# Optimization experiments

Measured on AMD Instinct MI355X. Metric: run time of the kernel, lower is better.

Reference implementation:

```python
import jax, jax.numpy as jnp
import numpy as np
import math

B, T = 8, 16
CODE_NUM = 1024
CODE_SIZE = 48
GRAPH_SIZE = 32
HIDDEN = 150      # hidden_size == t_output_size
T_ATTN = 32       # t_attention_size
DP_ATTN = 32      # DotProductAttention size
OUT = 1024


def _lin(k, fan_in, fan_out):
    s = 1.0 / math.sqrt(fan_in)
    kw, kb = jax.random.split(k)
    W = jax.random.uniform(kw, (fan_in, fan_out), minval=-s, maxval=s, dtype=jnp.float32)
    b = jax.random.uniform(kb, (fan_out,), minval=-s, maxval=s, dtype=jnp.float32)
    return W, b


def setup_inputs():
    key = jax.random.key(0)
    ks = jax.random.split(key, 16)
    u = jax.random.uniform(ks[0], (B, T, CODE_NUM))
    m1 = (u < 0.03).astype(jnp.float32)                   # persistent codes
    m2 = ((u >= 0.03) & (u < 0.05)).astype(jnp.float32)   # emerging neighbor codes
    m3 = ((u >= 0.05) & (u < 0.06)).astype(jnp.float32)   # emerging unrelated codes
    divided = jnp.stack([m1, m2, m3], axis=-1)            # [B,T,N,3], disjoint
    code_x = jnp.clip(m1 + m2 + m3, 0.0, 1.0)             # current-visit codes
    neighbors = ((u >= 0.06) & (u < 0.12)).astype(jnp.float32)
    lens = jax.random.randint(ks[1], (B,), T // 2, T + 1)
    a = (jax.random.uniform(ks[2], (CODE_NUM, CODE_NUM)) < 0.01).astype(jnp.float32)
    adj = a / (a.sum(axis=1, keepdims=True) + 1e-6)
    c_emb = jax.random.normal(ks[3], (CODE_NUM, CODE_SIZE)) * 0.05
    n_emb = jax.random.normal(ks[4], (CODE_NUM, CODE_SIZE)) * 0.05
    u_emb = jax.random.normal(ks[5], (CODE_NUM, GRAPH_SIZE)) * 0.05
    Wg, bg = _lin(ks[6], CODE_SIZE, GRAPH_SIZE)           # GraphLayer dense
    Wi, bi = _lin(ks[7], GRAPH_SIZE, 3 * HIDDEN)          # GRUCell input (r|z|n)
    Wh, bh = _lin(ks[8], HIDDEN, 3 * HIDDEN)              # GRUCell hidden (r|z|n)
    Wq, bq = _lin(ks[9], GRAPH_SIZE, T_ATTN)
    Wk, bk = _lin(ks[10], GRAPH_SIZE, T_ATTN)
    Wv, bv = _lin(ks[11], GRAPH_SIZE, HIDDEN)
    Wd, bd = _lin(ks[12], HIDDEN, DP_ATTN)                # DotProductAttention dense
    context = jax.random.normal(ks[13], (DP_ATTN,)) * 0.1
    Wc, bc = _lin(ks[14], HIDDEN, OUT)                    # Classifier
    return dict(code_x=code_x, divided=divided, neighbors=neighbors, lens=lens,
                adj=adj, c_emb=c_emb, n_emb=n_emb, u_emb=u_emb, Wg=Wg, bg=bg,
                Wi=Wi, bi=bi, Wh=Wh, bh=bh, Wq=Wq, bq=bq, Wk=Wk, bk=bk,
                Wv=Wv, bv=bv, Wd=Wd, bd=bd, context=context, Wc=Wc, bc=bc)


def _forward(code_x, divided, neighbors, lens, adj, c_emb, n_emb, u_emb,
             Wg, bg, Wi, bi, Wh, bh, Wq, bq, Wk, bk, Wv, bv, Wd, bd, context, Wc, bc):
    Bb, Tt, N = code_x.shape
    H = Wh.shape[0]
    NEG = -1e30
    scale = 1.0 / math.sqrt(Wq.shape[1])

    def step(carry, xs):
        h_prev, no_prev = carry                 # [B,N,H], [B,N,G]
        c_t, d_t, n_t, t_idx = xs               # [B,N], [B,N,3], [B,N], scalar
        c = c_t[..., None]
        nb = n_t[..., None]
        # GraphLayer: masked embeddings + one-hop adjacency aggregation
        ce = c * c_emb                           # [B,N,C]
        ne = nb * n_emb
        adj_ce = jnp.einsum('mn,bnc->bmc', adj, ce)
        adj_ne = jnp.einsum('mn,bnc->bmc', adj, ne)
        co = jax.nn.leaky_relu((ce + c * adj_ce + c * adj_ne) @ Wg + bg)      # [B,N,G]
        no = jax.nn.leaky_relu((ne + nb * adj_ne + nb * adj_ce) @ Wg + bg)

        m1 = d_t[..., 0]; m2 = d_t[..., 1]; m3 = d_t[..., 2]
        # TransitionLayer part 1: GRUCell on persistent (m1) codes; h_new starts at 0
        gi = co @ Wi + bi
        gh = h_prev @ Wh + bh
        i_r, i_z, i_n = jnp.split(gi, 3, axis=-1)
        h_r, h_z, h_n = jnp.split(gh, 3, axis=-1)
        r = jax.nn.sigmoid(i_r + h_r)
        z = jax.nn.sigmoid(i_z + h_z)
        n_g = jnp.tanh(i_n + r * h_n)
        h_m1 = (1.0 - z) * n_g + z * h_prev
        h_new = jnp.where(m1[..., None] > 0, h_m1, 0.0)

        # TransitionLayer part 2: single-head attention over emerging (m2|m3) codes, t>0
        m23 = (m2 + m3) > 0
        qrows = jnp.where(m2[..., None] > 0, no_prev,
                          jnp.where(m3[..., None] > 0, u_emb, 0.0))           # [B,N,G]
        q = qrows @ Wq + bq
        k = co @ Wk + bk
        v = qrows @ Wv + bv
        s = jnp.einsum('bia,bja->bij', q, k) * scale
        s = jnp.where(m23[:, None, :], s, NEG)   # keys restricted to m2|m3 set
        h_m23 = jnp.tanh(jnp.einsum('bij,bjh->bih', jax.nn.softmax(s, axis=-1), v))
        use23 = t_idx > 0
        h_new = jnp.where(jnp.logical_and(use23, m23)[..., None], h_m23, h_new)

        # per-step output: max-pool over each active subset (0 if subset empty)
        om1 = jnp.max(jnp.where(m1[..., None] > 0, h_m1, NEG), axis=1)
        om1 = jnp.where(jnp.any(m1 > 0, axis=1)[:, None], om1, 0.0)
        om23 = jnp.max(jnp.where(m23[..., None], h_m23, NEG), axis=1)
        om23 = jnp.where(jnp.logical_and(use23, jnp.any(m23, axis=1))[:, None], om23, 0.0)
        return (h_new, no), om1 + om23

    h0 = jnp.zeros((Bb, N, H), code_x.dtype)
    no0 = jnp.zeros((Bb, N, Wg.shape[1]), code_x.dtype)
    xs = (jnp.moveaxis(code_x, 1, 0), jnp.moveaxis(divided, 1, 0),
          jnp.moveaxis(neighbors, 1, 0), jnp.arange(Tt))
    _, outs = jax.lax.scan(step, (h0, no0), xs)
    outs = jnp.moveaxis(outs, 0, 1)              # [B,T,H]

    # DotProductAttention over (ragged) visit axis
    vu = (outs @ Wd + bd) @ context              # [B,T]
    tmask = jnp.arange(Tt)[None, :] < lens[:, None]
    score = jax.nn.softmax(jnp.where(tmask, vu, NEG), axis=-1)
    pooled = jnp.einsum('bth,bt->bh', outs, score)
    # Classifier (dropout_rate=0 -> identity) with sigmoid activation
    return jax.nn.sigmoid(pooled @ Wc + bc)


def reference(code_x, divided, neighbors, lens, adj, c_emb, n_emb, u_emb,
              Wg, bg, Wi, bi, Wh, bh, Wq, bq, Wk, bk, Wv, bv, Wd, bd, context, Wc, bc):
    return _forward(code_x, divided, neighbors, lens, adj, c_emb, n_emb, u_emb,
                    Wg, bg, Wi, bi, Wh, bh, Wq, bq, Wk, bk, Wv, bv, Wd, bd,
                    context, Wc, bc)
```

## Files before the change

kernel.cpp:

```cpp
#include <hip/hip_runtime.h>

#define Bq   8
#define Tq   16
#define Nq   1024
#define Cq   48
#define Gq   32
#define Hq   150
#define H3q  450
#define TAq  32
#define OUTq 1024
#define BTq  128
#define NBLK (2 * BTq)
#define THREADS 512

#define NC_CAP 128
#define NM_CAP 64
#define NACT   (2 * NC_CAP)
#define MTILE  16
#define NMH    (NM_CAP / 2)
#define CHUNK  16

__device__ __forceinline__ float lrelu(float x){ return x > 0.f ? x : 0.01f * x; }
__device__ __forceinline__ float sigm(float x){ return 1.f / (1.f + expf(-x)); }

__device__ __align__(16) int   g_n1[BTq], g_n23[BTq], g_nchain[BTq], g_nchain2[BTq];
__device__ __align__(16) int   g_list1[BTq][NM_CAP];
__device__ __align__(16) int   g_list23[BTq][NM_CAP];
__device__ __align__(16) int   g_mapc[BTq][Nq];
__device__ __align__(16) int   g_mapn[BTq][Nq];
__device__ __align__(16) int   g_chain[BTq][NM_CAP];
__device__ __align__(16) int   g_chain2[BTq][NM_CAP];
__device__ __align__(16) int   g_cls[BTq][NM_CAP];
__device__ __align__(16) float g_co[BTq][NC_CAP][Gq];
__device__ __align__(16) float g_no[BTq][NC_CAP][Gq];
__device__ __align__(16) float g_hm23[BTq][NM_CAP][Hq];
__device__ __align__(16) float g_om23p2[2][BTq][Hq];
__device__ __align__(16) float g_hm1[BTq][NM_CAP][Hq];
__device__ __align__(16) float g_om1p2[2][BTq][Hq];
__device__ __align__(16) float g_om1c[BTq][Hq];

template<typename T>
__device__ __forceinline__ T gld(const T* p){
    return __hip_atomic_load(p, __ATOMIC_RELAXED, __HIP_MEMORY_SCOPE_AGENT);
}
template<typename T>
__device__ __forceinline__ void gst(T* p, T v){
    __hip_atomic_store(p, v, __ATOMIC_RELAXED, __HIP_MEMORY_SCOPE_AGENT);
}

__device__ unsigned int g_done[NBLK][16];

__device__ __forceinline__ void publish(unsigned int val){
    asm volatile("s_waitcnt vmcnt(0)" ::: "memory");
    __syncthreads();
    if (threadIdx.x == 0)
        __hip_atomic_store(&g_done[blockIdx.x][0], val,
                           __ATOMIC_RELAXED, __HIP_MEMORY_SCOPE_AGENT);
}

__device__ __forceinline__ void spin_ge(int b2, unsigned int tgt){
    while ((int)(__hip_atomic_load(&g_done[b2][0],
                                   __ATOMIC_RELAXED, __HIP_MEMORY_SCOPE_AGENT) - tgt) < 0)
        __builtin_amdgcn_s_sleep(4);
}

__device__ __forceinline__ void gi3(const float* co_row, const float* Wi, const float* bi, int h,
                                    float& gr, float& gz, float& gn){
    gr = bi[h]; gz = bi[Hq + h]; gn = bi[2 * Hq + h];
    #pragma unroll
    for (int g = 0; g < Gq; ++g){
        float c = co_row[g];
        const float* w = Wi + g * H3q + h;
        gr += c * w[0];
        gz += c * w[Hq];
        gn += c * w[2 * Hq];
    }
}

#define WARM(ptr, nfloats) { int nv_ = (nfloats) >> 2; \
    for (int i4_ = blk * THREADS + tid; i4_ < nv_; i4_ += NBLK * THREADS){ \
        float4 v_ = ((const float4*)(ptr))[i4_]; \
        wacc += v_.x + v_.y + v_.z + v_.w; } }

union SharedU {
    struct {
        unsigned char cf[Nq], nf[Nq];
        short lc[NC_CAP], ln[NC_CAP];
        short act[NACT];
        float Wg[Cq][Gq];
        float Pact[NACT][Gq];
        float A[MTILE][NACT];
    } co;
    struct {
        unsigned char f1[Nq], f2[Nq], f3[Nq];
        short l1[NM_CAP], l23[NM_CAP];
        unsigned char wm[NMH];
        float co23[NM_CAP][Gq];
        float qr[NM_CAP][Gq];
        float q[NMH][TAq + 1];
        float k[NM_CAP][TAq + 1];
        float s[NMH][NM_CAP + 1];
        float vv[NM_CAP][Hq];
        float hm[NMH][Hq];
    } mid;
    struct {
        short map1p[Nq], map23p[Nq];
        short l1[NM_CAP];
        unsigned char cls[NM_CAP];
        int   m23l[NM_CAP];
        float co1[NMH][Gq];
        float hb[Hq];
        float ghf[H3q];
        float gi[NMH][H3q];
    } g1;
    struct {
        int   proc[NM_CAP];
        float hb[CHUNK][Hq];
        float co[CHUNK][Gq];
        float ghf[CHUNK][H3q];
        float hm[CHUNK][Hq];
        float cmax[Hq];
    } g1b;
    struct {
        int   nch2[Tq];
        float co[Gq];
        float hb[Hq];
        float ghf[H3q];
        float outs[Tq][Hq];
        float wdc[Hq];
        float score[Tq];
        float pooled[Hq];
        float cpart[32][17];
    } fin;
};

#define CO_PREFETCH(P, kk) { int rbase_ = half + (kk) * 2 * MTILE; \
    int ntile_ = min(MTILE, (total - rbase_ + 1) / 2); int lim_ = ntile_ * total; \
    _Pragma("unroll") for (int u = 0; u < 8; ++u){ int idx_ = tid + u * THREADS; \
        if (idx_ < lim_){ int ti_ = idx_ / total, j_ = idx_ - ti_ * total; \
            P[u] = adj[(size_t)sh.co.act[rbase_ + 2 * ti_] * Nq + sh.co.act[j_]]; } } }

#define CO_STORE(P, kk) { int rbase_ = half + (kk) * 2 * MTILE; \
    int ntile_ = min(MTILE, (total - rbase_ + 1) / 2); int lim_ = ntile_ * total; \
    _Pragma("unroll") for (int u = 0; u < 8; ++u){ int idx_ = tid + u * THREADS; \
        if (idx_ < lim_){ int ti_ = idx_ / total, j_ = idx_ - ti_ * total; \
            sh.co.A[ti_][j_] = P[u]; } } }

#define CO_COMPUTE(kk) { int rbase_ = half + (kk) * 2 * MTILE; \
    int ntile_ = min(MTILE, (total - rbase_ + 1) / 2); \
    if (grp < ntile_){ int r_ = rbase_ + 2 * grp; float agg_ = 0.f; \
        _Pragma("unroll 4") for (int j_ = 0; j_ < total; ++j_) \
            agg_ += sh.co.A[grp][j_] * sh.co.Pact[j_][g]; \
        float v_ = lrelu(sh.co.Pact[r_][g] + agg_ + bgv); \
        if (r_ < nc) gst(&g_co[bt][r_][g], v_); else gst(&g_no[bt][r_ - nc][g], v_); } }

__global__ __launch_bounds__(THREADS, 1) void k_fused(
    const float* code_x, const float* divided, const float* neighbors,
    const int* lens, const float* adj, const float* c_emb, const float* n_emb,
    const float* u_emb, const float* Wg, const float* bg,
    const float* Wi, const float* bi, const float* Wh, const float* bh,
    const float* Wq_, const float* bq_, const float* Wk_, const float* bk_,
    const float* Wv_, const float* bv_, const float* Wd, const float* bd,
    const float* ctx, const float* Wc, const float* bc, float* out)
{
    __shared__ SharedU sh;
    __shared__ int s_n0, s_n1v, s_i2;
    const int tid = threadIdx.x;
    const int blk = blockIdx.x;
    const int bt   = blk >> 1;
    const int half = blk & 1;
    const int t    = bt % Tq;
    const int btp  = bt - 1;
    const unsigned int bar0 = __hip_atomic_load(&g_done[blk][0],
                                                __ATOMIC_RELAXED, __HIP_MEMORY_SCOPE_AGENT);

    float wacc = 0.f;
    WARM(code_x,    BTq * Nq);
    WARM(neighbors, BTq * Nq);
    WARM(adj,       Nq * Nq);
    WARM(divided,   BTq * Nq * 3);
    WARM(c_emb,     Nq * Cq);
    WARM(n_emb,     Nq * Cq);
    WARM(u_emb,     Nq * Gq);
    WARM(Wi,        Gq * H3q);
    WARM(Wh,        Hq * H3q);
    WARM(Wc,        Hq * OUTq);
    WARM(Wv_,       Gq * Hq);
    WARM(Wd,        Hq * TAq);

    {
        int wave = tid >> 6, lane = tid & 63;
        for (int n = tid; n < Nq; n += THREADS){
            sh.co.cf[n] = (code_x[bt * Nq + n]    > 0.f) ? 1 : 0;
            sh.co.nf[n] = (neighbors[bt * Nq + n] > 0.f) ? 1 : 0;
        }
        for (int i = tid; i < Cq * Gq; i += THREADS) (&sh.co.Wg[0][0])[i] = Wg[i];
        __syncthreads();
        if (wave == 0){
            int base = 0;
            for (int start = 0; start < Nq; start += 64){
                int n = start + lane;
                int pred = sh.co.cf[n];
                unsigned long long mm = __ballot(pred != 0);
                int pos = base + (int)__popcll(mm & ((1ull << lane) - 1ull));
                if (pred && pos < NC_CAP) sh.co.lc[pos] = (short)n;
                base += (int)__popcll(mm);
            }
            if (lane == 0) s_n0 = min(base, NC_CAP);
        } else if (wave == 1){
            int base = 0;
            for (int start = 0; start < Nq; start += 64){
                int n = start + lane;
                int pred = sh.co.nf[n];
                unsigned long long mm = __ballot(pred != 0);
                int pos = base + (int)__popcll(mm & ((1ull << lane) - 1ull));
                if (pred && pos < NC_CAP) sh.co.ln[pos] = (short)n;
                base += (int)__popcll(mm);
            }
            if (lane == 0) s_n1v = min(base, NC_CAP);
        } else {
            if (half == 0) for (int n = tid - 128; n < Nq; n += 384) gst(&g_mapc[bt][n], -1);
            else           for (int n = tid - 128; n < Nq; n += 384) gst(&g_mapn[bt][n], -1);
        }
        __syncthreads();
        int nc = s_n0, nn = s_n1v, total = nc + nn;

        for (int i = tid; i < total; i += THREADS) sh.co.act[i] = (i < nc) ? sh.co.lc[i] : sh.co.ln[i - nc];
        if (half == 0) for (int i = tid; i < nc; i += THREADS) gst(&g_mapc[bt][sh.co.lc[i]], i);
        else           for (int i = tid; i < nn; i += THREADS) gst(&g_mapn[bt][sh.co.ln[i]], i);
        __syncthreads();

        for (int idx = tid; idx < total * Gq; idx += THREADS){
            int i = idx >> 5, g = idx & 31;
            int row = sh.co.act[i];
            const float* e = (i < nc) ? (c_emb + row * Cq) : (n_emb + row * Cq);
            float acc = 0.f;
            #pragma unroll
            for (int c = 0; c < Cq; ++c) acc += e[c] * sh.co.Wg[c][g];
            sh.co.Pact[i][g] = acc;
        }
        __syncthreads();

        int g = tid & 31, grp = tid >> 5;
        float bgv = bg[g];
        int ntiles = (total > half) ? (total - half + 2 * MTILE - 1) / (2 * MTILE) : 0;
        float pA[8], pB[8];
        if (ntiles > 0) CO_PREFETCH(pA, 0);
        for (int k = 0; k < ntiles; ){
            CO_STORE(pA, k);
            __syncthreads();
            if (k + 1 < ntiles) CO_PREFETCH(pB, k + 1);
            CO_COMPUTE(k);
            __syncthreads();
            ++k; if (k >= ntiles) break;
            CO_STORE(pB, k);
            __syncthreads();
            if (k + 1 < ntiles) CO_PREFETCH(pA, k + 1);
            CO_COMPUTE(k);
            __syncthreads();
            ++k;
        }
    }
    asm volatile("" :: "v"(wacc));
    publish(bar0 + 1);
    float dv[6];
    #pragma unroll
    for (int u = 0; u < 6; ++u) dv[u] = divided[(size_t)bt * (Nq * 3) + tid + u * THREADS];
    if (tid == 0) spin_ge(blk ^ 1, bar0 + 1);
    else if (t > 0 && tid == 1) spin_ge(2 * btp,     bar0 + 1);
    else if (t > 0 && tid == 2) spin_ge(2 * btp + 1, bar0 + 1);
    __syncthreads();

    {
        int wave = tid >> 6, lane = tid & 63;
        #pragma unroll
        for (int u = 0; u < 6; ++u){
            int idx = tid + u * THREADS;
            int n = idx / 3, c = idx - n * 3;
            unsigned char f = (dv[u] > 0.f) ? 1 : 0;
            if (c == 0) sh.mid.f1[n] = f;
            else if (c == 1) sh.mid.f2[n] = f;
            else sh.mid.f3[n] = f;
        }
        __syncthreads();
        if (wave == 0){
            int base = 0;
            for (int start = 0; start < Nq; start += 64){
                int n = start + lane;
                int pred = sh.mid.f1[n];
                unsigned long long mm = __ballot(pred != 0);
                int pos = base + (int)__popcll(mm & ((1ull << lane) - 1ull));
                if (pred && pos < NM_CAP) sh.mid.l1[pos] = (short)n;
                base += (int)__popcll(mm);
            }
            if (lane == 0) s_n0 = min(base, NM_CAP);
        } else if (wave == 1){
            int base = 0;
            for (int start = 0; start < Nq; start += 64){
                int n = start + lane;
                int m2 = sh.mid.f2[n], m3 = sh.mid.f3[n];
                int pred = m2 | m3;
                unsigned long long mm = __ballot(pred != 0);
                int pos = base + (int)__popcll(mm & ((1ull << lane) - 1ull));
                if (pred && pos < NM_CAP) sh.mid.l23[pos] = (short)(n | (m2 ? 0x400 : 0));
                base += (int)__popcll(mm);
            }
            if (lane == 0) s_n1v = min(base, NM_CAP);
        }
        __syncthreads();
        int n1 = s_n0, n23 = s_n1v;
        if (half == 0){
            for (int i = tid; i < n1;  i += THREADS) gst(&g_list1[bt][i],  (int)sh.mid.l1[i]);
            for (int i = tid; i < n23; i += THREADS) gst(&g_list23[bt][i], (int)sh.mid.l23[i]);
            if (tid == 0){ gst(&g_n1[bt], n1); gst(&g_n23[bt], n23); }
        }
        if (t != 0 && n23 != 0){
            int nMy = (n23 > half) ? ((n23 - half + 1) >> 1) : 0;

            for (int il = tid; il < nMy; il += THREADS){
                int row = sh.mid.l23[2 * il + half] & 1023;
                unsigned char wmv = 0;
                if (t < Tq - 1) wmv = (divided[((size_t)(bt + 1) * Nq + row) * 3] > 0.f) ? 1 : 0;
                sh.mid.wm[il] = wmv;
            }
            for (int idx = tid; idx < n23 * Gq; idx += THREADS){
                int i = idx >> 5, g = idx & 31;
                sh.mid.co23[i][g] = gld(&g_co[bt][gld(&g_mapc[bt][sh.mid.l23[i] & 1023])][g]);
            }
            for (int idx = tid; idx < n23 * Gq; idx += THREADS){
                int i = idx >> 5, g = idx & 31;
                int e = sh.mid.l23[i], row = e & 1023;
                float qv;
                if (e & 0x400){
                    int slot = gld(&g_mapn[btp][row]);
                    qv = (slot >= 0) ? gld(&g_no[btp][slot][g]) : lrelu(bg[g]);
                } else {
                    qv = u_emb[row * Gq + g];
                }
                sh.mid.qr[i][g] = qv;
            }
            __syncthreads();
            for (int idx = tid; idx < n23 * TAq; idx += THREADS){
                int i = idx >> 5, a = idx & 31;
                float acck = bk_[a];
                #pragma unroll
                for (int g = 0; g < Gq; ++g) acck += sh.mid.co23[i][g] * Wk_[g * TAq + a];
                sh.mid.k[i][a] = acck;
            }
            for (int idx = tid; idx < nMy * TAq; idx += THREADS){
                int il = idx >> 5, a = idx & 31;
                int i = 2 * il + half;
                float accq = bq_[a];
                #pragma unroll
                for (int g = 0; g < Gq; ++g) accq += sh.mid.qr[i][g] * Wq_[g * TAq + a];
                sh.mid.q[il][a] = accq;
            }
            for (int idx = tid; idx < n23 * Hq; idx += THREADS){
                int i = idx / Hq, h = idx % Hq;
                float acc = bv_[h];
                #pragma unroll
                for (int g = 0; g < Gq; ++g) acc += sh.mid.qr[i][g] * Wv_[g * Hq + h];
                sh.mid.vv[i][h] = acc;
            }
            __syncthreads();

            const float scale = 0.17677669529663687f;
            for (int idx = tid; idx < nMy * n23; idx += THREADS){
                int il = idx / n23, j = idx % n23;
                float acc = 0.f;
                #pragma unroll
                for (int a = 0; a < TAq; ++a) acc += sh.mid.q[il][a] * sh.mid.k[j][a];
                sh.mid.s[il][j] = acc * scale;
            }
            __syncthreads();
            for (int il = tid; il < nMy; il += THREADS){
                float mx = -1e30f;
                for (int j = 0; j < n23; ++j) mx = fmaxf(mx, sh.mid.s[il][j]);
                float sum = 0.f;
                for (int j = 0; j < n23; ++j){ float e = expf(sh.mid.s[il][j] - mx); sh.mid.s[il][j] = e; sum += e; }
                float inv = 1.f / sum;
                for (int j = 0; j < n23; ++j) sh.mid.s[il][j] *= inv;
            }
            __syncthreads();
            for (int idx = tid; idx < nMy * Hq; idx += THREADS){
                int il = idx / Hq, h = idx % Hq;
                float acc = 0.f;
                for (int j = 0; j < n23; ++j) acc += sh.mid.s[il][j] * sh.mid.vv[j][h];
                sh.mid.hm[il][h] = tanhf(acc);
            }
            __syncthreads();
            for (int idx = tid; idx < nMy * Hq; idx += THREADS){
                int il = idx / Hq, h = idx % Hq;
                if (sh.mid.wm[il]) gst(&g_hm23[bt][2 * il + half][h], sh.mid.hm[il][h]);
            }
            for (int h = tid; h < Hq; h += THREADS){
                float mx = -1e30f;
                for (int il = 0; il < nMy; ++il) mx = fmaxf(mx, sh.mid.hm[il][h]);
                gst(&g_om23p2[half][bt][h], mx);
            }
        }
    }
    publish(bar0 + 2);
    if (tid == 0) spin_ge(blk ^ 1, bar0 + 2);
    else if (t > 0 && tid == 1) spin_ge(2 * btp,     bar0 + 2);
    else if (t > 0 && tid == 2) spin_ge(2 * btp + 1, bar0 + 2);
    __syncthreads();

    {
        int n1 = gld(&g_n1[bt]);
        int nMy = (n1 > half) ? ((n1 - half + 1) >> 1) : 0;
        for (int n = tid; n < Nq; n += THREADS){
            if (t >= 1) sh.g1.map1p[n] = -1;
            if (t >= 2) sh.g1.map23p[n] = -1;
        }
        for (int i = tid; i < n1; i += THREADS) sh.g1.l1[i] = (short)gld(&g_list1[bt][i]);
        __syncthreads();
        if (t >= 1){
            int n1p = gld(&g_n1[btp]);
            for (int i = tid; i < n1p; i += THREADS) sh.g1.map1p[gld(&g_list1[btp][i])] = (short)i;
            if (t >= 2){
                int n23p = gld(&g_n23[btp]);
                for (int i = tid; i < n23p; i += THREADS) sh.g1.map23p[gld(&g_list23[btp][i]) & 1023] = (short)i;
            }
        }
        __syncthreads();
        if (tid < 64){
            int i = tid;
            int cls = 0, sp = -1;
            if (i < n1 && t >= 1){
                int row = sh.g1.l1[i];
                if (sh.g1.map1p[row] >= 0){ cls = 1; sp = sh.g1.map1p[row]; }
                else if (t >= 2 && sh.g1.map23p[row] >= 0){ cls = 2; sp = sh.g1.map23p[row]; }
            }
            if (i < n1) sh.g1.cls[i] = (unsigned char)cls;
            if (half == 0 && i < n1) gst(&g_cls[bt][i], cls);
            unsigned long long mch = __ballot(cls == 1);
            unsigned long long m23 = __ballot(cls == 2 && (i & 1) == half);
            int pch = (int)__popcll(mch & ((1ull << i) - 1ull));
            int p23 = (int)__popcll(m23 & ((1ull << i) - 1ull));
            if (half == 0 && cls == 1) gst(&g_chain[bt][pch], (i << 16) | sp);
            if (cls == 2 && (i & 1) == half) sh.g1.m23l[p23] = (i << 16) | sp;
            if (i == 0){
                s_i2 = (int)__popcll(m23);
                if (half == 0) gst(&g_nchain[bt], (int)__popcll(mch));
            }
        }
        for (int idx = tid; idx < nMy * Gq; idx += THREADS){
            int il = idx >> 5, g = idx & 31;
            sh.g1.co1[il][g] = gld(&g_co[bt][gld(&g_mapc[bt][sh.g1.l1[2 * il + half]])][g]);
        }
        __syncthreads();

        if (tid < H3q){
            float wcol[Gq];
            #pragma unroll
            for (int g = 0; g < Gq; ++g) wcol[g] = Wi[g * H3q + tid];
            float bij = bi[tid];
            for (int il = 0; il < nMy; ++il){
                float acc = bij;
                #pragma unroll
                for (int g = 0; g < Gq; ++g) acc += sh.g1.co1[il][g] * wcol[g];
                sh.g1.gi[il][tid] = acc;
            }
        }
        __syncthreads();

        for (int idx = tid; idx < nMy * Hq; idx += THREADS){
            int il = idx / Hq, h = idx % Hq;
            int i = 2 * il + half;
            if (sh.g1.cls[i] != 0) continue;
            float gr = sh.g1.gi[il][h], gz = sh.g1.gi[il][Hq + h], gn = sh.g1.gi[il][2 * Hq + h];
            float r  = sigm(gr + bh[h]);
            float z  = sigm(gz + bh[Hq + h]);
            float ng = tanhf(gn + r * bh[2 * Hq + h]);
            sh.g1.gi[il][h] = (1.f - z) * ng;
        }
        __syncthreads();

        int nf23 = s_i2;
        for (int f = 0; f < nf23; ++f){
            int pk = sh.g1.m23l[f]; int i = pk >> 16, sp = pk & 0xffff;
            int il = i >> 1;
            for (int h = tid; h < Hq; h += THREADS) sh.g1.hb[h] = gld(&g_hm23[btp][sp][h]);
            __syncthreads();
            for (int j = tid; j < H3q; j += THREADS){
                float acc = bh[j];
                for (int k2 = 0; k2 < Hq; ++k2) acc += sh.g1.hb[k2] * Wh[k2 * H3q + j];
                sh.g1.ghf[j] = acc;
            }
            __syncthreads();
            for (int h = tid; h < Hq; h += THREADS){
                float gr = sh.g1.gi[il][h], gz = sh.g1.gi[il][Hq + h], gn = sh.g1.gi[il][2 * Hq + h];
                float r  = sigm(gr + sh.g1.ghf[h]);
                float z  = sigm(gz + sh.g1.ghf[Hq + h]);
                float ng = tanhf(gn + r * sh.g1.ghf[2 * Hq + h]);
                sh.g1.gi[il][h] = (1.f - z) * ng + z * sh.g1.hb[h];
            }
            __syncthreads();
        }

        for (int idx = tid; idx < nMy * Hq; idx += THREADS){
            int il = idx / Hq, h = idx % Hq;
            int i = 2 * il + half;
            if (sh.g1.cls[i] != 1) gst(&g_hm1[bt][i][h], sh.g1.gi[il][h]);
        }
        for (int h = tid; h < Hq; h += THREADS){
            float mx = -1e30f;
            for (int il = 0; il < nMy; ++il)
                if (sh.g1.cls[2 * il + half] != 1) mx = fmaxf(mx, sh.g1.gi[il][h]);
            gst(&g_om1p2[half][bt][h], mx);
        }
    }
    publish(bar0 + 3);

    if (half == 0){
        if (t > 0){
            if (tid == 0) spin_ge(2 * btp,     bar0 + 3);
            else if (tid == 1) spin_ge(2 * btp + 1, bar0 + 3);
        }
        __syncthreads();
        {
            int nch = (t > 0) ? gld(&g_nchain[bt]) : 0;
            for (int h = tid; h < Hq; h += THREADS) sh.g1b.cmax[h] = -1e30f;
            if (tid < 64){
                int c = tid;
                int pk = 0, defer = 0;
                if (c < nch){
                    pk = gld(&g_chain[bt][c]);
                    int sp = pk & 0xffff;
                    defer = (gld(&g_cls[btp][sp]) == 1) ? 1 : 0;
                }
                unsigned long long md = __ballot((c < nch) && defer);
                unsigned long long mp = __ballot((c < nch) && !defer);
                int pos  = (int)__popcll(md & ((1ull << c) - 1ull));
                int ppos = (int)__popcll(mp & ((1ull << c) - 1ull));
                if ((c < nch) && defer)  gst(&g_chain2[bt][pos], pk);
                if ((c < nch) && !defer) sh.g1b.proc[ppos] = pk;
                if (c == 0){
                    gst(&g_nchain2[bt], (int)__popcll(md));
                    s_i2 = (int)__popcll(mp);
                }
            }
            __syncthreads();
            int nproc = s_i2;
            for (int cb = 0; cb < nproc; cb += CHUNK){
                int nc2 = min(CHUNK, nproc - cb);
                for (int idx = tid; idx < nc2 * Hq; idx += THREADS){
                    int c = idx / Hq, h = idx % Hq;
                    int sp = sh.g1b.proc[cb + c] & 0xffff;
                    sh.g1b.hb[c][h] = gld(&g_hm1[btp][sp][h]);
                }
                for (int idx = tid; idx < nc2 * Gq; idx += THREADS){
                    int c = idx >> 5, g = idx & 31;
                    int i = sh.g1b.proc[cb + c] >> 16;
                    sh.g1b.co[c][g] = gld(&g_co[bt][gld(&g_mapc[bt][gld(&g_list1[bt][i])])][g]);
                }
                __syncthreads();
                for (int idx = tid; idx < nc2 * H3q; idx += THREADS){
                    int c = idx / H3q, j = idx - c * H3q;
                    float acc = bh[j];
                    for (int k2 = 0; k2 < Hq; ++k2) acc += sh.g1b.hb[c][k2] * Wh[k2 * H3q + j];
                    sh.g1b.ghf[c][j] = acc;
                }
                __syncthreads();
                for (int idx = tid; idx < nc2 * Hq; idx += THREADS){
                    int c = idx / Hq, h = idx % Hq;
                    int i = sh.g1b.proc[cb + c] >> 16;
                    float gr, gz, gn;
                    gi3(sh.g1b.co[c], Wi, bi, h, gr, gz, gn);
                    float r  = sigm(gr + sh.g1b.ghf[c][h]);
                    float z  = sigm(gz + sh.g1b.ghf[c][Hq + h]);
                    float ng = tanhf(gn + r * sh.g1b.ghf[c][2 * Hq + h]);
                    float v  = (1.f - z) * ng + z * sh.g1b.hb[c][h];
                    gst(&g_hm1[bt][i][h], v);
                    sh.g1b.hm[c][h] = v;
                }
                __syncthreads();
                for (int h = tid; h < Hq; h += THREADS){
                    float mx = sh.g1b.cmax[h];
                    for (int c = 0; c < nc2; ++c) mx = fmaxf(mx, sh.g1b.hm[c][h]);
                    sh.g1b.cmax[h] = mx;
                }
                __syncthreads();
            }
            for (int h = tid; h < Hq; h += THREADS) gst(&g_om1c[bt][h], sh.g1b.cmax[h]);
        }
        publish(bar0 + 4);

        if ((blk & 31) == 0){
            int b = blk >> 5;
            if (tid < 16) spin_ge(32 * b + 2 * tid, bar0 + 4);
            __syncthreads();
            if (tid < Tq) sh.fin.nch2[tid] = (tid > 0) ? gld(&g_nchain2[b * Tq + tid]) : 0;
            __syncthreads();
            for (int tt = 1; tt < Tq; ++tt){
                int bt2 = b * Tq + tt, btp2 = bt2 - 1;
                int nch2 = sh.fin.nch2[tt];
                for (int c = 0; c < nch2; ++c){
                    int pk = gld(&g_chain2[bt2][c]); int i = pk >> 16, sp = pk & 0xffff;
                    if (tid < Gq) sh.fin.co[tid] = gld(&g_co[bt2][gld(&g_mapc[bt2][gld(&g_list1[bt2][i])])][tid]);
                    for (int h = tid; h < Hq; h += THREADS) sh.fin.hb[h] = gld(&g_hm1[btp2][sp][h]);
                    __syncthreads();
                    for (int j = tid; j < H3q; j += THREADS){
                        float acc = bh[j];
                        for (int k2 = 0; k2 < Hq; ++k2) acc += sh.fin.hb[k2] * Wh[k2 * H3q + j];
                        sh.fin.ghf[j] = acc;
                    }
                    __syncthreads();
                    for (int h = tid; h < Hq; h += THREADS){
                        float gr, gz, gn;
                        gi3(sh.fin.co, Wi, bi, h, gr, gz, gn);
                        float r  = sigm(gr + sh.fin.ghf[h]);
                        float z  = sigm(gz + sh.fin.ghf[Hq + h]);
                        float ng = tanhf(gn + r * sh.fin.ghf[2 * Hq + h]);
                        gst(&g_hm1[bt2][i][h], (1.f - z) * ng + z * sh.fin.hb[h]);
                    }
                    __syncthreads();
                }
            }
            publish(bar0 + 5);
        }
    }

    {
        int b = blk >> 5;
        if (tid == 0) spin_ge(32 * b, bar0 + 5);
        else if (tid >= 1 && tid < 17) spin_ge(32 * b + 2 * (tid - 1) + 1, bar0 + 3);
        __syncthreads();

        if (tid < Tq) sh.fin.nch2[tid] = (tid > 0) ? gld(&g_nchain2[b * Tq + tid]) : 0;
        __syncthreads();
        for (int idx = tid; idx < Tq * Hq; idx += THREADS){
            int tt = idx / Hq, h = idx % Hq;
            int bt2 = b * Tq + tt;
            int n1 = gld(&g_n1[bt2]), n23 = (tt > 0) ? gld(&g_n23[bt2]) : 0;
            float o = 0.f;
            if (n1 > 0){
                float mx = fmaxf(fmaxf(gld(&g_om1p2[0][bt2][h]), gld(&g_om1p2[1][bt2][h])),
                                 gld(&g_om1c[bt2][h]));
                int nd = sh.fin.nch2[tt];
                for (int c = 0; c < nd; ++c){
                    int i = gld(&g_chain2[bt2][c]) >> 16;
                    mx = fmaxf(mx, gld(&g_hm1[bt2][i][h]));
                }
                o = mx;
            }
            if (n23 > 0) o += fmaxf(gld(&g_om23p2[0][bt2][h]), gld(&g_om23p2[1][bt2][h]));
            sh.fin.outs[tt][h] = o;
        }
        for (int h = tid; h < Hq; h += THREADS){
            float acc = 0.f;
            for (int d = 0; d < 32; ++d) acc += Wd[h * 32 + d] * ctx[d];
            sh.fin.wdc[h] = acc;
        }
        __syncthreads();
        int len = lens[b];
        if (tid < Tq){
            int tt = tid;
            float acc = 0.f;
            for (int d = 0; d < 32; ++d) acc += bd[d] * ctx[d];
            for (int h = 0; h < Hq; ++h) acc += sh.fin.outs[tt][h] * sh.fin.wdc[h];
            sh.fin.score[tt] = (tt < len) ? acc : -1e30f;
        }
        __syncthreads();
        if (tid == 0){
            float mx = -1e30f;
            for (int tt = 0; tt < Tq; ++tt) mx = fmaxf(mx, sh.fin.score[tt]);
            float sum = 0.f;
            for (int tt = 0; tt < Tq; ++tt){ float e = expf(sh.fin.score[tt] - mx); sh.fin.score[tt] = e; sum += e; }
            float inv = 1.f / sum;
            for (int tt = 0; tt < Tq; ++tt) sh.fin.score[tt] *= inv;
        }
        __syncthreads();
        for (int h = tid; h < Hq; h += THREADS){
            float acc = 0.f;
            for (int tt = 0; tt < Tq; ++tt) acc += sh.fin.score[tt] * sh.fin.outs[tt][h];
            sh.fin.pooled[h] = acc;
        }
        __syncthreads();
        int obase = (blk & 31) * 32;
        {
            int ol = tid & 31, seg = tid >> 5;
            int h0 = seg * 10, h1 = min(Hq, h0 + 10);
            float acc = 0.f;
            for (int h = h0; h < h1; ++h) acc += sh.fin.pooled[h] * Wc[h * OUTq + obase + ol];
            sh.fin.cpart[ol][seg] = acc;
        }
        __syncthreads();
        if (tid < 32){
            int o = obase + tid;
            float acc = bc[o];
            #pragma unroll
            for (int s2 = 0; s2 < 16; ++s2) acc += sh.fin.cpart[tid][s2];
            out[b * OUTq + o] = sigm(acc);
        }
    }
    publish(bar0 + 6);
}

extern "C" void kernel_launch(void* const* d_in, const int* in_sizes, int n_in,
                              void* d_out, int out_size, void* d_ws, size_t ws_size,
                              hipStream_t stream){
    const float* code_x    = (const float*)d_in[0];
    const float* divided   = (const float*)d_in[1];
    const float* neighbors = (const float*)d_in[2];
    const int*   lens      = (const int*)  d_in[3];
    const float* adj       = (const float*)d_in[4];
    const float* c_emb     = (const float*)d_in[5];
    const float* n_emb     = (const float*)d_in[6];
    const float* u_emb     = (const float*)d_in[7];
    const float* Wg        = (const float*)d_in[8];
    const float* bg        = (const float*)d_in[9];
    const float* Wi        = (const float*)d_in[10];
    const float* bi        = (const float*)d_in[11];
    const float* Wh        = (const float*)d_in[12];
    const float* bh        = (const float*)d_in[13];
    const float* Wq_       = (const float*)d_in[14];
    const float* bq_       = (const float*)d_in[15];
    const float* Wk_       = (const float*)d_in[16];
    const float* bk_       = (const float*)d_in[17];
    const float* Wv_       = (const float*)d_in[18];
    const float* bv_       = (const float*)d_in[19];
    const float* Wd_       = (const float*)d_in[20];
    const float* bd_       = (const float*)d_in[21];
    const float* ctx       = (const float*)d_in[22];
    const float* Wc_       = (const float*)d_in[23];
    const float* bc_       = (const float*)d_in[24];
    float* out = (float*)d_out;

    hipLaunchKernelGGL(k_fused, dim3(NBLK), dim3(THREADS), 0, stream,
                       code_x, divided, neighbors, lens, adj, c_emb, n_emb, u_emb,
                       Wg, bg, Wi, bi, Wh, bh, Wq_, bq_, Wk_, bk_, Wv_, bv_,
                       Wd_, bd_, ctx, Wc_, bc_, out);
}
```

Before: 233.3 us.

## Split each visit across four blocks instead of two

Doubles the grid so that each (batch, visit) pair is handled by four cooperating blocks rather than two. Row work in the graph layer, attention and GRU stages is interleaved by index mod 4, and the partial max buffers and spin-wait barriers grow to four slots. Launch bounds allow four blocks per CU, and a shared-memory union is added to shrink the per-block footprint. The aim is more parallelism per serial stage; the cost is more inter-block barrier traffic, duplicated setup work, and the need for all 512 persistent blocks to be co-resident.

```diff
diff --git a/kernel.cpp b/kernel.cpp
--- a/kernel.cpp
+++ b/kernel.cpp
@@ -10,14 +10,14 @@
 #define TAq  32
 #define OUTq 1024
 #define BTq  128
-#define NBLK (2 * BTq)
+#define NBLK (4 * BTq)
 #define THREADS 512
 
 #define NC_CAP 128
 #define NM_CAP 64
 #define NACT   (2 * NC_CAP)
 #define MTILE  16
-#define NMH    (NM_CAP / 2)
+#define NMH4   (NM_CAP / 4)
 #define CHUNK  16
 
 __device__ __forceinline__ float lrelu(float x){ return x > 0.f ? x : 0.01f * x; }
@@ -34,9 +34,9 @@
 __device__ __align__(16) float g_co[BTq][NC_CAP][Gq];
 __device__ __align__(16) float g_no[BTq][NC_CAP][Gq];
 __device__ __align__(16) float g_hm23[BTq][NM_CAP][Hq];
-__device__ __align__(16) float g_om23p2[2][BTq][Hq];
+__device__ __align__(16) float g_om23p4[4][BTq][Hq];
 __device__ __align__(16) float g_hm1[BTq][NM_CAP][Hq];
-__device__ __align__(16) float g_om1p2[2][BTq][Hq];
+__device__ __align__(16) float g_om1p4[4][BTq][Hq];
 __device__ __align__(16) float g_om1c[BTq][Hq];
 
 template<typename T>
@@ -94,24 +94,25 @@
     struct {
         unsigned char f1[Nq], f2[Nq], f3[Nq];
         short l1[NM_CAP], l23[NM_CAP];
-        unsigned char wm[NMH];
-        float co23[NM_CAP][Gq];
-        float qr[NM_CAP][Gq];
-        float q[NMH][TAq + 1];
+        unsigned char wm[NMH4];
+        union {
+            struct { float co23[NM_CAP][Gq]; float qr[NM_CAP][Gq]; } in;
+            float hm[NMH4][Hq];
+        } u;
+        float q[NMH4][TAq + 1];
         float k[NM_CAP][TAq + 1];
-        float s[NMH][NM_CAP + 1];
+        float s[NMH4][NM_CAP + 1];
         float vv[NM_CAP][Hq];
-        float hm[NMH][Hq];
     } mid;
     struct {
         short map1p[Nq], map23p[Nq];
         short l1[NM_CAP];
         unsigned char cls[NM_CAP];
         int   m23l[NM_CAP];
-        float co1[NMH][Gq];
+        float co1[NMH4][Gq];
         float hb[Hq];
         float ghf[H3q];
-        float gi[NMH][H3q];
+        float gi[NMH4][H3q];
     } g1;
     struct {
         int   proc[NM_CAP];
@@ -130,31 +131,31 @@
         float wdc[Hq];
         float score[Tq];
         float pooled[Hq];
-        float cpart[32][17];
+        float cpart[16][33];
     } fin;
 };
 
-#define CO_PREFETCH(P, kk) { int rbase_ = half + (kk) * 2 * MTILE; \
-    int ntile_ = min(MTILE, (total - rbase_ + 1) / 2); int lim_ = ntile_ * total; \
+#define CO_PREFETCH(P, kk) { int rbase_ = qtr + (kk) * 4 * MTILE; \
+    int ntile_ = min(MTILE, (total - rbase_ + 3) / 4); int lim_ = ntile_ * total; \
     _Pragma("unroll") for (int u = 0; u < 8; ++u){ int idx_ = tid + u * THREADS; \
         if (idx_ < lim_){ int ti_ = idx_ / total, j_ = idx_ - ti_ * total; \
-            P[u] = adj[(size_t)sh.co.act[rbase_ + 2 * ti_] * Nq + sh.co.act[j_]]; } } }
-
-#define CO_STORE(P, kk) { int rbase_ = half + (kk) * 2 * MTILE; \
-    int ntile_ = min(MTILE, (total - rbase_ + 1) / 2); int lim_ = ntile_ * total; \
+            P[u] = adj[(size_t)sh.co.act[rbase_ + 4 * ti_] * Nq + sh.co.act[j_]]; } } }
+
+#define CO_STORE(P, kk) { int rbase_ = qtr + (kk) * 4 * MTILE; \
+    int ntile_ = min(MTILE, (total - rbase_ + 3) / 4); int lim_ = ntile_ * total; \
     _Pragma("unroll") for (int u = 0; u < 8; ++u){ int idx_ = tid + u * THREADS; \
         if (idx_ < lim_){ int ti_ = idx_ / total, j_ = idx_ - ti_ * total; \
             sh.co.A[ti_][j_] = P[u]; } } }
 
-#define CO_COMPUTE(kk) { int rbase_ = half + (kk) * 2 * MTILE; \
-    int ntile_ = min(MTILE, (total - rbase_ + 1) / 2); \
-    if (grp < ntile_){ int r_ = rbase_ + 2 * grp; float agg_ = 0.f; \
+#define CO_COMPUTE(kk) { int rbase_ = qtr + (kk) * 4 * MTILE; \
+    int ntile_ = min(MTILE, (total - rbase_ + 3) / 4); \
+    if (grp < ntile_){ int r_ = rbase_ + 4 * grp; float agg_ = 0.f; \
         _Pragma("unroll 4") for (int j_ = 0; j_ < total; ++j_) \
             agg_ += sh.co.A[grp][j_] * sh.co.Pact[j_][g]; \
         float v_ = lrelu(sh.co.Pact[r_][g] + agg_ + bgv); \
         if (r_ < nc) gst(&g_co[bt][r_][g], v_); else gst(&g_no[bt][r_ - nc][g], v_); } }
 
-__global__ __launch_bounds__(THREADS, 1) void k_fused(
+__global__ __launch_bounds__(THREADS, 4) void k_fused(
     const float* code_x, const float* divided, const float* neighbors,
     const int* lens, const float* adj, const float* c_emb, const float* n_emb,
     const float* u_emb, const float* Wg, const float* bg,
@@ -167,8 +168,9 @@
     __shared__ int s_n0, s_n1v, s_i2;
     const int tid = threadIdx.x;
     const int blk = blockIdx.x;
-    const int bt   = blk >> 1;
-    const int half = blk & 1;
+    const int bt   = blk >> 2;
+    const int qtr  = blk & 3;
+    const int sb   = blk & ~3;
     const int t    = bt % Tq;
     const int btp  = bt - 1;
     const unsigned int bar0 = __hip_atomic_load(&g_done[blk][0],
@@ -219,15 +221,15 @@
             }
             if (lane == 0) s_n1v = min(base, NC_CAP);
         } else {
-            if (half == 0) for (int n = tid - 128; n < Nq; n += 384) gst(&g_mapc[bt][n], -1);
-            else           for (int n = tid - 128; n < Nq; n += 384) gst(&g_mapn[bt][n], -1);
+            if (qtr == 0)      for (int n = tid - 128; n < Nq; n += 384) gst(&g_mapc[bt][n], -1);
+            else if (qtr == 1) for (int n = tid - 128; n < Nq; n += 384) gst(&g_mapn[bt][n], -1);
         }
         __syncthreads();
         int nc = s_n0, nn = s_n1v, total = nc + nn;
 
         for (int i = tid; i < total; i += THREADS) sh.co.act[i] = (i < nc) ? sh.co.lc[i] : sh.co.ln[i - nc];
-        if (half == 0) for (int i = tid; i < nc; i += THREADS) gst(&g_mapc[bt][sh.co.lc[i]], i);
-        else           for (int i = tid; i < nn; i += THREADS) gst(&g_mapn[bt][sh.co.ln[i]], i);
+        if (qtr == 0)      for (int i = tid; i < nc; i += THREADS) gst(&g_mapc[bt][sh.co.lc[i]], i);
+        else if (qtr == 1) for (int i = tid; i < nn; i += THREADS) gst(&g_mapn[bt][sh.co.ln[i]], i);
         __syncthreads();
 
         for (int idx = tid; idx < total * Gq; idx += THREADS){
@@ -243,7 +245,7 @@
 
         int g = tid & 31, grp = tid >> 5;
         float bgv = bg[g];
-        int ntiles = (total > half) ? (total - half + 2 * MTILE - 1) / (2 * MTILE) : 0;
+        int ntiles = (total > qtr) ? (total - qtr + 4 * MTILE - 1) / (4 * MTILE) : 0;
         float pA[8], pB[8];
         if (ntiles > 0) CO_PREFETCH(pA, 0);
         for (int k = 0; k < ntiles; ){
@@ -266,9 +268,8 @@
     float dv[6];
     #pragma unroll
     for (int u = 0; u < 6; ++u) dv[u] = divided[(size_t)bt * (Nq * 3) + tid + u * THREADS];
-    if (tid == 0) spin_ge(blk ^ 1, bar0 + 1);
-    else if (t > 0 && tid == 1) spin_ge(2 * btp,     bar0 + 1);
-    else if (t > 0 && tid == 2) spin_ge(2 * btp + 1, bar0 + 1);
+    if (tid < 4 && tid != qtr) spin_ge(sb + tid, bar0 + 1);
+    if (t > 0 && tid >= 4 && tid < 8) spin_ge(4 * btp + (tid - 4), bar0 + 1);
     __syncthreads();
 
     {
@@ -309,23 +310,23 @@
         }
         __syncthreads();
         int n1 = s_n0, n23 = s_n1v;
-        if (half == 0){
+        if (qtr == 0){
             for (int i = tid; i < n1;  i += THREADS) gst(&g_list1[bt][i],  (int)sh.mid.l1[i]);
             for (int i = tid; i < n23; i += THREADS) gst(&g_list23[bt][i], (int)sh.mid.l23[i]);
             if (tid == 0){ gst(&g_n1[bt], n1); gst(&g_n23[bt], n23); }
         }
         if (t != 0 && n23 != 0){
-            int nMy = (n23 > half) ? ((n23 - half + 1) >> 1) : 0;
+            int nMy = (n23 > qtr) ? ((n23 - qtr + 3) >> 2) : 0;
 
             for (int il = tid; il < nMy; il += THREADS){
-                int row = sh.mid.l23[2 * il + half] & 1023;
+                int row = sh.mid.l23[4 * il + qtr] & 1023;
                 unsigned char wmv = 0;
                 if (t < Tq - 1) wmv = (divided[((size_t)(bt + 1) * Nq + row) * 3] > 0.f) ? 1 : 0;
                 sh.mid.wm[il] = wmv;
             }
             for (int idx = tid; idx < n23 * Gq; idx += THREADS){
                 int i = idx >> 5, g = idx & 31;
-                sh.mid.co23[i][g] = gld(&g_co[bt][gld(&g_mapc[bt][sh.mid.l23[i] & 1023])][g]);
+                sh.mid.u.in.co23[i][g] = gld(&g_co[bt][gld(&g_mapc[bt][sh.mid.l23[i] & 1023])][g]);
             }
             for (int idx = tid; idx < n23 * Gq; idx += THREADS){
                 int i = idx >> 5, g = idx & 31;
@@ -337,29 +338,29 @@
                 } else {
                     qv = u_emb[row * Gq + g];
                 }
-                sh.mid.qr[i][g] = qv;
+                sh.mid.u.in.qr[i][g] = qv;
             }
             __syncthreads();
             for (int idx = tid; idx < n23 * TAq; idx += THREADS){
                 int i = idx >> 5, a = idx & 31;
                 float acck = bk_[a];
                 #pragma unroll
-                for (int g = 0; g < Gq; ++g) acck += sh.mid.co23[i][g] * Wk_[g * TAq + a];
+                for (int g = 0; g < Gq; ++g) acck += sh.mid.u.in.co23[i][g] * Wk_[g * TAq + a];
                 sh.mid.k[i][a] = acck;
             }
             for (int idx = tid; idx < nMy * TAq; idx += THREADS){
                 int il = idx >> 5, a = idx & 31;
-                int i = 2 * il + half;
+                int i = 4 * il + qtr;
                 float accq = bq_[a];
                 #pragma unroll
-                for (int g = 0; g < Gq; ++g) accq += sh.mid.qr[i][g] * Wq_[g * TAq + a];
+                for (int g = 0; g < Gq; ++g) accq += sh.mid.u.in.qr[i][g] * Wq_[g * TAq + a];
                 sh.mid.q[il][a] = accq;
             }
             for (int idx = tid; idx < n23 * Hq; idx += THREADS){
                 int i = idx / Hq, h = idx % Hq;
                 float acc = bv_[h];
                 #pragma unroll
-                for (int g = 0; g < Gq; ++g) acc += sh.mid.qr[i][g] * Wv_[g * Hq + h];
+                for (int g = 0; g < Gq; ++g) acc += sh.mid.u.in.qr[i][g] * Wv_[g * Hq + h];
                 sh.mid.vv[i][h] = acc;
             }
             __syncthreads();
@@ -386,29 +387,28 @@
                 int il = idx / Hq, h = idx % Hq;
                 float acc = 0.f;
                 for (int j = 0; j < n23; ++j) acc += sh.mid.s[il][j] * sh.mid.vv[j][h];
-                sh.mid.hm[il][h] = tanhf(acc);
+                sh.mid.u.hm[il][h] = tanhf(acc);
             }
             __syncthreads();
             for (int idx = tid; idx < nMy * Hq; idx += THREADS){
                 int il = idx / Hq, h = idx % Hq;
-                if (sh.mid.wm[il]) gst(&g_hm23[bt][2 * il + half][h], sh.mid.hm[il][h]);
+                if (sh.mid.wm[il]) gst(&g_hm23[bt][4 * il + qtr][h], sh.mid.u.hm[il][h]);
             }
             for (int h = tid; h < Hq; h += THREADS){
                 float mx = -1e30f;
-                for (int il = 0; il < nMy; ++il) mx = fmaxf(mx, sh.mid.hm[il][h]);
-                gst(&g_om23p2[half][bt][h], mx);
+                for (int il = 0; il < nMy; ++il) mx = fmaxf(mx, sh.mid.u.hm[il][h]);
+                gst(&g_om23p4[qtr][bt][h], mx);
             }
         }
     }
     publish(bar0 + 2);
-    if (tid == 0) spin_ge(blk ^ 1, bar0 + 2);
-    else if (t > 0 && tid == 1) spin_ge(2 * btp,     bar0 + 2);
-    else if (t > 0 && tid == 2) spin_ge(2 * btp + 1, bar0 + 2);
+    if (tid < 4 && tid != qtr) spin_ge(sb + tid, bar0 + 2);
+    if (t > 0 && tid >= 4 && tid < 8) spin_ge(4 * btp + (tid - 4), bar0 + 2);
     __syncthreads();
 
     {
         int n1 = gld(&g_n1[bt]);
-        int nMy = (n1 > half) ? ((n1 - half + 1) >> 1) : 0;
+        int nMy = (n1 > qtr) ? ((n1 - qtr + 3) >> 2) : 0;
         for (int n = tid; n < Nq; n += THREADS){
             if (t >= 1) sh.g1.map1p[n] = -1;
             if (t >= 2) sh.g1.map23p[n] = -1;
@@ -433,21 +433,21 @@
                 else if (t >= 2 && sh.g1.map23p[row] >= 0){ cls = 2; sp = sh.g1.map23p[row]; }
             }
             if (i < n1) sh.g1.cls[i] = (unsigned char)cls;
-            if (half == 0 && i < n1) gst(&g_cls[bt][i], cls);
+            if (qtr == 0 && i < n1) gst(&g_cls[bt][i], cls);
             unsigned long long mch = __ballot(cls == 1);
-            unsigned long long m23 = __ballot(cls == 2 && (i & 1) == half);
+            unsigned long long m23 = __ballot(cls == 2 && (i & 3) == qtr);
             int pch = (int)__popcll(mch & ((1ull << i) - 1ull));
             int p23 = (int)__popcll(m23 & ((1ull << i) - 1ull));
-            if (half == 0 && cls == 1) gst(&g_chain[bt][pch], (i << 16) | sp);
-            if (cls == 2 && (i & 1) == half) sh.g1.m23l[p23] = (i << 16) | sp;
+            if (qtr == 0 && cls == 1) gst(&g_chain[bt][pch], (i << 16) | sp);
+            if (cls == 2 && (i & 3) == qtr) sh.g1.m23l[p23] = (i << 16) | sp;
             if (i == 0){
                 s_i2 = (int)__popcll(m23);
-                if (half == 0) gst(&g_nchain[bt], (int)__popcll(mch));
+                if (qtr == 0) gst(&g_nchain[bt], (int)__popcll(mch));
             }
         }
         for (int idx = tid; idx < nMy * Gq; idx += THREADS){
             int il = idx >> 5, g = idx & 31;
-            sh.g1.co1[il][g] = gld(&g_co[bt][gld(&g_mapc[bt][sh.g1.l1[2 * il + half]])][g]);
+            sh.g1.co1[il][g] = gld(&g_co[bt][gld(&g_mapc[bt][sh.g1.l1[4 * il + qtr]])][g]);
         }
         __syncthreads();
 
@@ -467,7 +467,7 @@
 
         for (int idx = tid; idx < nMy * Hq; idx += THREADS){
             int il = idx / Hq, h = idx % Hq;
-            int i = 2 * il + half;
+            int i = 4 * il + qtr;
             if (sh.g1.cls[i] != 0) continue;
             float gr = sh.g1.gi[il][h], gz = sh.g1.gi[il][Hq + h], gn = sh.g1.gi[il][2 * Hq + h];
             float r  = sigm(gr + bh[h]);
@@ -480,7 +480,7 @@
         int nf23 = s_i2;
         for (int f = 0; f < nf23; ++f){
             int pk = sh.g1.m23l[f]; int i = pk >> 16, sp = pk & 0xffff;
-            int il = i >> 1;
+            int il = i >> 2;
             for (int h = tid; h < Hq; h += THREADS) sh.g1.hb[h] = gld(&g_hm23[btp][sp][h]);
             __syncthreads();
             for (int j = tid; j < H3q; j += THREADS){
@@ -501,22 +501,21 @@
 
         for (int idx = tid; idx < nMy * Hq; idx += THREADS){
             int il = idx / Hq, h = idx % Hq;
-            int i = 2 * il + half;
+            int i = 4 * il + qtr;
             if (sh.g1.cls[i] != 1) gst(&g_hm1[bt][i][h], sh.g1.gi[il][h]);
         }
         for (int h = tid; h < Hq; h += THREADS){
             float mx = -1e30f;
             for (int il = 0; il < nMy; ++il)
-                if (sh.g1.cls[2 * il + half] != 1) mx = fmaxf(mx, sh.g1.gi[il][h]);
-            gst(&g_om1p2[half][bt][h], mx);
+                if (sh.g1.cls[4 * il + qtr] != 1) mx = fmaxf(mx, sh.g1.gi[il][h]);
+            gst(&g_om1p4[qtr][bt][h], mx);
         }
     }
     publish(bar0 + 3);
 
-    if (half == 0){
+    if (qtr == 0){
         if (t > 0){
-            if (tid == 0) spin_ge(2 * btp,     bar0 + 3);
-            else if (tid == 1) spin_ge(2 * btp + 1, bar0 + 3);
+            if (tid < 4) spin_ge(4 * btp + tid, bar0 + 3);
         }
         __syncthreads();
         {
@@ -587,9 +586,9 @@
         }
         publish(bar0 + 4);
 
-        if ((blk & 31) == 0){
-            int b = blk >> 5;
-            if (tid < 16) spin_ge(32 * b + 2 * tid, bar0 + 4);
+        if ((blk & 63) == 0){
+            int b = blk >> 6;
+            if (tid < 16) spin_ge(64 * b + 4 * tid, bar0 + 4);
             __syncthreads();
             if (tid < Tq) sh.fin.nch2[tid] = (tid > 0) ? gld(&g_nchain2[b * Tq + tid]) : 0;
             __syncthreads();
@@ -623,9 +622,13 @@
     }
 
     {
-        int b = blk >> 5;
-        if (tid == 0) spin_ge(32 * b, bar0 + 5);
-        else if (tid >= 1 && tid < 17) spin_ge(32 * b + 2 * (tid - 1) + 1, bar0 + 3);
+        int b = blk >> 6;
+        if (tid == 0) spin_ge(64 * b, bar0 + 5);
+        else if (tid >= 1 && tid < 49){
+            int idx = tid - 1;
+            int tt = idx / 3, qq = 1 + idx % 3;
+            spin_ge(64 * b + 4 * tt + qq, bar0 + 3);
+        }
         __syncthreads();
 
         if (tid < Tq) sh.fin.nch2[tid] = (tid > 0) ? gld(&g_nchain2[b * Tq + tid]) : 0;
@@ -636,8 +639,9 @@
             int n1 = gld(&g_n1[bt2]), n23 = (tt > 0) ? gld(&g_n23[bt2]) : 0;
             float o = 0.f;
             if (n1 > 0){
-                float mx = fmaxf(fmaxf(gld(&g_om1p2[0][bt2][h]), gld(&g_om1p2[1][bt2][h])),
-                                 gld(&g_om1c[bt2][h]));
+                float mx = fmaxf(fmaxf(gld(&g_om1p4[0][bt2][h]), gld(&g_om1p4[1][bt2][h])),
+                                 fmaxf(gld(&g_om1p4[2][bt2][h]), gld(&g_om1p4[3][bt2][h])));
+                mx = fmaxf(mx, gld(&g_om1c[bt2][h]));
                 int nd = sh.fin.nch2[tt];
                 for (int c = 0; c < nd; ++c){
                     int i = gld(&g_chain2[bt2][c]) >> 16;
@@ -645,7 +649,11 @@
                 }
                 o = mx;
             }
-            if (n23 > 0) o += fmaxf(gld(&g_om23p2[0][bt2][h]), gld(&g_om23p2[1][bt2][h]));
+            if (n23 > 0){
+                float m23x = fmaxf(fmaxf(gld(&g_om23p4[0][bt2][h]), gld(&g_om23p4[1][bt2][h])),
+                                   fmaxf(gld(&g_om23p4[2][bt2][h]), gld(&g_om23p4[3][bt2][h])));
+                o += m23x;
+            }
             sh.fin.outs[tt][h] = o;
         }
         for (int h = tid; h < Hq; h += THREADS){
@@ -678,20 +686,20 @@
             sh.fin.pooled[h] = acc;
         }
         __syncthreads();
-        int obase = (blk & 31) * 32;
+        int obase = (blk & 63) * 16;
         {
-            int ol = tid & 31, seg = tid >> 5;
-            int h0 = seg * 10, h1 = min(Hq, h0 + 10);
+            int ol = tid & 15, seg = tid >> 4;
+            int h0 = seg * 5, h1 = min(Hq, h0 + 5);
             float acc = 0.f;
             for (int h = h0; h < h1; ++h) acc += sh.fin.pooled[h] * Wc[h * OUTq + obase + ol];
             sh.fin.cpart[ol][seg] = acc;
         }
         __syncthreads();
-        if (tid < 32){
+        if (tid < 16){
             int o = obase + tid;
             float acc = bc[o];
             #pragma unroll
-            for (int s2 = 0; s2 < 16; ++s2) acc += sh.fin.cpart[tid][s2];
+            for (int s2 = 0; s2 < 32; ++s2) acc += sh.fin.cpart[tid][s2];
             out[b * OUTq + o] = sigm(acc);
         }
     }
```

Result: slower. 281.9 us (+20.8%).
